# Performance work log

Hardware: AMD Instinct MI355X
Metric: run time of the kernel (lower is better)

## Reference

```python
import jax, jax.numpy as jnp
import numpy as np

C = 256          # in_channels == out_channels
L = 131072       # sequence length (multiple of BL)
BL = 64          # dilation == sliding-attention block length
CQ = C // 2      # q/k channels (r1=2)
CV = C // 2      # v channels (r2=2)
ALPHA = 1.0
EPS_IN = 1e-5    # InstanceNorm eps


def setup_inputs() -> dict:
    key = jax.random.key(0)
    ks = jax.random.split(key, 16)
    s = 0.05
    return {
        "x": jax.random.normal(ks[0], (1, C, L), jnp.float32),
        "f": jax.random.normal(ks[1], (1, C, L), jnp.float32),
        "mask": jnp.ones((1, 1, L), jnp.float32),
        # ConvFeedForward: Conv1d(C, C, 3, padding=BL, dilation=BL)
        "Wff": jax.random.normal(ks[2], (C, C, 3), jnp.float32) * s,
        "bff": jax.random.normal(ks[3], (C,), jnp.float32) * s,
        # AttLayer 1x1 convs
        "Wq": jax.random.normal(ks[4], (CQ, C), jnp.float32) * s,
        "bq": jax.random.normal(ks[5], (CQ,), jnp.float32) * s,
        "Wk": jax.random.normal(ks[6], (CQ, C), jnp.float32) * s,
        "bk": jax.random.normal(ks[7], (CQ,), jnp.float32) * s,
        "Wv": jax.random.normal(ks[8], (CV, C), jnp.float32) * s,
        "bv": jax.random.normal(ks[9], (CV,), jnp.float32) * s,
        "Wo": jax.random.normal(ks[10], (C, CV), jnp.float32) * s,
        "bo": jax.random.normal(ks[11], (C,), jnp.float32) * s,
        # AttModule.conv_1x1
        "Wc": jax.random.normal(ks[12], (C, C), jnp.float32) * s,
        "bc": jax.random.normal(ks[13], (C,), jnp.float32) * s,
    }


def _conv1x1(W, b, x):  # x: (B, Cin, L)
    return jnp.einsum('oc,bcl->bol', W, x) + b[None, :, None]


def _forward(x, f, mask, Wff, bff, Wq, bq, Wk, bk, Wv, bv, Wo, bo, Wc, bc):
    # --- ConvFeedForward: dilated conv + ReLU (same-length output) ---
    out = jax.lax.conv_general_dilated(
        x, Wff, window_strides=(1,), padding=[(BL, BL)], rhs_dilation=(BL,),
        dimension_numbers=('NCH', 'OIH', 'NCH')) + bff[None, :, None]
    out = jax.nn.relu(out)  # (1, C, L)

    # --- InstanceNorm1d (affine=False, biased var) ---
    mu = out.mean(axis=-1, keepdims=True)
    var = out.var(axis=-1, keepdims=True)
    xn = (out - mu) * jax.lax.rsqrt(var + EPS_IN)

    # --- AttLayer (sliding_att, decoder: value from f) ---
    q = _conv1x1(Wq, bq, xn)   # (1, CQ, L)
    k = _conv1x1(Wk, bk, xn)   # (1, CQ, L)
    v = _conv1x1(Wv, bv, f)    # (1, CV, L)

    nb = L // BL
    half = BL // 2
    pm = mask[:, 0:1, :]                         # (1,1,L) padding mask
    # pad halo of BL//2 zeros on each side of k, v, padding_mask
    kp = jnp.pad(k, ((0, 0), (0, 0), (half, half)))
    vp = jnp.pad(v, ((0, 0), (0, 0), (half, half)))
    mp = jnp.pad(pm, ((0, 0), (0, 0), (half, half)))
    # window index: block i sees [i*BL, i*BL + 2*BL) of the padded sequence
    idx = jnp.arange(nb)[:, None] * BL + jnp.arange(2 * BL)[None, :]  # (nb, 2BL)
    kw = kp[:, :, idx]   # (1, CQ, nb, 2BL)
    vw = vp[:, :, idx]   # (1, CV, nb, 2BL)
    mw = mp[:, 0, idx]   # (1, nb, 2BL)

    # window mask: query i attends keys [i, i+BL) within the 2BL window
    d = jnp.arange(2 * BL)[None, :] - jnp.arange(BL)[:, None]
    wm = ((d >= 0) & (d < BL)).astype(x.dtype)          # (BL, 2BL)
    fm = wm[None, None] * mw[:, :, None, :]             # (1, nb, BL, 2BL)

    qb = q.reshape(1, CQ, nb, BL)
    energy = jnp.einsum('bcnl,bcnm->bnlm', qb, kw) / np.sqrt(CQ).astype(x.dtype)
    att = jax.nn.softmax(energy + jnp.log(fm + 1e-6), axis=-1) * fm
    ov = jnp.einsum('bcnm,bnlm->bcnl', vw, att)         # (1, CV, nb, BL)
    oo = jnp.einsum('oc,bcnl->bonl', Wo, jax.nn.relu(ov)) + bo[None, :, None, None]
    att_out = oo.reshape(1, C, L) * pm                  # (1, C, L)

    # --- scaled residual + 1x1 conv + (dropout=identity) + masked residual ---
    h = ALPHA * att_out + out
    h = _conv1x1(Wc, bc, h)
    return (x + h) * mask


def reference(x, f, mask, Wff, bff, Wq, bq, Wk, bk, Wv, bv, Wo, bo, Wc, bc):
    return _forward(x, f, mask, Wff, bff, Wq, bq, Wk, bk, Wv, bv, Wo, bo, Wc, bc)
```

## Files before the change

kernel.cpp:

```cpp
#include <hip/hip_runtime.h>

#define L_LEN 131072
#define NB    2048
#define NT    1024

typedef unsigned short u16;
typedef __attribute__((ext_vector_type(4))) float f32x4;
typedef __attribute__((ext_vector_type(8))) short s16x8;
typedef __attribute__((ext_vector_type(4))) short s16x4;

#define WS_OUTT  0ull
#define WS_QT    67108864ull
#define WS_PSUM  100663296ull
#define WS_PSQ   101711872ull
#define WS_MEAN  102760448ull
#define WS_RSTD  102761472ull
#define WS_WFFB  102762496ull
#define WS_WQKB  103155712ull
#define WS_WVB   103286784ull
#define WS_WOB   103352320ull
#define WS_WCB   103417856ull
#define WS_BQKP  103548928ull

__device__ __forceinline__ u16 f2bf(float v){
  union { float f; unsigned u; } a; a.f = v;
  unsigned r = a.u + 0x7fffu + ((a.u >> 16) & 1u);
  return (u16)(r >> 16);
}
__device__ __forceinline__ float bf2f(u16 u){
  union { unsigned u; float f; } a; a.u = ((unsigned)u) << 16; return a.f;
}
__device__ __forceinline__ f32x4 mfma16(s16x8 a, s16x8 b, f32x4 c){
  return __builtin_amdgcn_mfma_f32_16x16x32_bf16(a, b, c, 0, 0, 0);
}
__device__ __forceinline__ s16x8 ld8(const void* p){ return *(const s16x8*)p; }

__global__ __launch_bounds__(256) void k_prep(
    const float* __restrict__ Wff, const float* __restrict__ Wv,
    const float* __restrict__ Wo,  const float* __restrict__ Wc,
    short* __restrict__ wffb, short* __restrict__ wvb,
    short* __restrict__ wob,  short* __restrict__ wcb)
{
  int i = blockIdx.x * 256 + threadIdx.x;
  if (i < 196608){
    int o = i / 768, kk = i % 768;
    int t = kk >> 8, c = kk & 255;
    wffb[i] = (short)f2bf(Wff[(o*256 + c)*3 + t]);
  } else if (i < 229376){ int j = i - 196608; wvb[j] = (short)f2bf(Wv[j]); }
  else if (i < 262144){ int j = i - 229376; wob[j] = (short)f2bf(Wo[j]); }
  else if (i < 327680){ int j = i - 262144; wcb[j] = (short)f2bf(Wc[j]); }
}

__global__ __launch_bounds__(512, 4) void k_conv(
    const float* __restrict__ x, const short* __restrict__ wffb,
    const float* __restrict__ bff, u16* __restrict__ outT,
    float* __restrict__ psum, float* __restrict__ psq)
{
  __shared__ u16 bl[128*40];
  const int wg = blockIdx.x, l0 = wg * 128;
  const int tid = threadIdx.x;
  const int w = tid >> 6, lane = tid & 63, p = lane & 15, g = lane >> 4;
  const int cS = tid >> 4, posq = tid & 15;
  f32x4 acc[2][8] = {};
  #pragma unroll 1
  for (int ks = 0; ks < 24; ++ks){
    const int t = ks >> 3, c0 = (ks & 7) * 32;
    {
      const int gbase = l0 + 64*(t-1) + posq*8;
      float vv[8];
      if (gbase >= 0 && gbase <= L_LEN - 8){
        const f32x4* sp = (const f32x4*)(x + (size_t)(c0 + cS)*L_LEN + gbase);
        f32x4 a0 = sp[0], a1 = sp[1];
        vv[0]=a0[0];vv[1]=a0[1];vv[2]=a0[2];vv[3]=a0[3];
        vv[4]=a1[0];vv[5]=a1[1];vv[6]=a1[2];vv[7]=a1[3];
      } else {
        #pragma unroll
        for (int u = 0; u < 8; ++u) vv[u] = 0.f;
      }
      const int col = cS ^ ((posq & 3) << 3);
      #pragma unroll
      for (int u = 0; u < 8; ++u) bl[(posq*8 + u)*40 + col] = f2bf(vv[u]);
    }
    __syncthreads();
    s16x8 af[2];
    af[0] = ld8(wffb + (size_t)(32*w +      p)*768 + ks*32 + 8*g);
    af[1] = ld8(wffb + (size_t)(32*w + 16 + p)*768 + ks*32 + 8*g);
    #pragma unroll
    for (int fn = 0; fn < 8; ++fn){
      const int r = 16*fn + p;
      s16x8 b = ld8(&bl[r*40 + ((8*g) ^ (((r>>3)&3)<<3))]);
      acc[0][fn] = mfma16(af[0], b, acc[0][fn]);
      acc[1][fn] = mfma16(af[1], b, acc[1][fn]);
    }
    __syncthreads();
  }
  #pragma unroll
  for (int fm = 0; fm < 2; ++fm){
    const int o0 = 32*w + 16*fm + 4*g;
    float ssum[4] = {0,0,0,0}, ssq[4] = {0,0,0,0};
    #pragma unroll
    for (int fn = 0; fn < 8; ++fn){
      s16x4 pk;
      #pragma unroll
      for (int i = 0; i < 4; ++i){
        float val = fmaxf(acc[fm][fn][i] + bff[o0+i], 0.f);
        pk[i] = (short)f2bf(val);
        ssum[i] += val; ssq[i] += val*val;
      }
      *(s16x4*)(outT + (size_t)(l0 + 16*fn + p)*256 + o0) = pk;
    }
    #pragma unroll
    for (int i = 0; i < 4; ++i){
      float a = ssum[i], b = ssq[i];
      #pragma unroll
      for (int d = 1; d < 16; d <<= 1){ a += __shfl_xor(a, d, 16); b += __shfl_xor(b, d, 16); }
      if (p == 0){ psum[(size_t)(o0+i)*NT + wg] = a; psq[(size_t)(o0+i)*NT + wg] = b; }
    }
  }
}

__global__ __launch_bounds__(256) void k_stats(
    const float* __restrict__ psum, const float* __restrict__ psq,
    float* __restrict__ mean, float* __restrict__ rstd)
{
  __shared__ float ss[256], sq[256];
  const int ch = blockIdx.x, tid = threadIdx.x;
  float a = 0.f, b = 0.f;
  for (int j = tid; j < NT; j += 256){ a += psum[(size_t)ch*NT + j]; b += psq[(size_t)ch*NT + j]; }
  ss[tid] = a; sq[tid] = b;
  __syncthreads();
  for (int st = 128; st > 0; st >>= 1){
    if (tid < st){ ss[tid] += ss[tid+st]; sq[tid] += sq[tid+st]; }
    __syncthreads();
  }
  if (tid == 0){
    float m = ss[0] / (float)L_LEN;
    float v = sq[0] / (float)L_LEN - m*m;
    mean[ch] = m;
    rstd[ch] = rsqrtf(v + 1e-5f);
  }
}

__global__ __launch_bounds__(256) void k_adj(
    const float* __restrict__ Wq, const float* __restrict__ Wk,
    const float* __restrict__ bq, const float* __restrict__ bk,
    const float* __restrict__ mean, const float* __restrict__ rstd,
    short* __restrict__ wqkb, float* __restrict__ bqkp)
{
  __shared__ float red[256];
  const int o = blockIdx.x, c = threadIdx.x;
  const float* src = (o < 128) ? (Wq + (size_t)o*256) : (Wk + (size_t)(o-128)*256);
  const float bias = (o < 128) ? bq[o] : bk[o-128];
  float wv = src[c] * rstd[c];
  wqkb[o*256 + c] = (short)f2bf(wv);
  red[c] = wv * mean[c];
  __syncthreads();
  for (int st = 128; st > 0; st >>= 1){
    if (c < st) red[c] += red[c+st];
    __syncthreads();
  }
  if (c == 0) bqkp[o] = bias - red[0];
}

__global__ __launch_bounds__(256, 4) void k_v(
    const float* __restrict__ fin, const short* __restrict__ wvb,
    const float* __restrict__ bv, u16* __restrict__ vout)
{
  __shared__ u16 bl[128*40];
  const int wg = blockIdx.x, l0 = wg * 128;
  const int tid = threadIdx.x;
  const int w = tid >> 6, lane = tid & 63, p = lane & 15, g = lane >> 4;
  const int posq = tid & 15;
  f32x4 acc[2][8] = {};
  #pragma unroll 1
  for (int ks = 0; ks < 8; ++ks){
    #pragma unroll
    for (int rep = 0; rep < 2; ++rep){
      const int c = rep*16 + (tid >> 4);
      const f32x4* sp = (const f32x4*)(fin + (size_t)(ks*32 + c)*L_LEN + l0 + posq*8);
      f32x4 a0 = sp[0], a1 = sp[1];
      float vv[8] = {a0[0],a0[1],a0[2],a0[3],a1[0],a1[1],a1[2],a1[3]};
      const int col = c ^ ((posq & 3) << 3);
      #pragma unroll
      for (int u = 0; u < 8; ++u) bl[(posq*8 + u)*40 + col] = f2bf(vv[u]);
    }
    __syncthreads();
    s16x8 af[2];
    af[0] = ld8(wvb + (size_t)(32*w +      p)*256 + ks*32 + 8*g);
    af[1] = ld8(wvb + (size_t)(32*w + 16 + p)*256 + ks*32 + 8*g);
    #pragma unroll
    for (int fn = 0; fn < 8; ++fn){
      const int r = 16*fn + p;
      s16x8 b = ld8(&bl[r*40 + ((8*g) ^ (((r>>3)&3)<<3))]);
      acc[0][fn] = mfma16(af[0], b, acc[0][fn]);
      acc[1][fn] = mfma16(af[1], b, acc[1][fn]);
    }
    __syncthreads();
  }
  #pragma unroll
  for (int fm = 0; fm < 2; ++fm){
    #pragma unroll
    for (int fn = 0; fn < 8; ++fn){
      #pragma unroll
      for (int i = 0; i < 4; ++i){
        const int cv = 32*w + 16*fm + 4*g + i;
        vout[(size_t)cv*L_LEN + l0 + 16*fn + p] = f2bf(acc[fm][fn][i] + bv[cv]);
      }
    }
  }
}

__global__ __launch_bounds__(512, 4) void k_qk(
    const u16* __restrict__ outT, const short* __restrict__ wqkb,
    const float* __restrict__ bqkp, u16* __restrict__ qT, u16* __restrict__ kT)
{
  extern __shared__ u16 tile[];
  const int wg = blockIdx.x, l0 = wg * 128;
  const int tid = threadIdx.x;
  const int w = tid >> 6, lane = tid & 63, p = lane & 15, g = lane >> 4;
  #pragma unroll
  for (int rep = 0; rep < 8; ++rep){
    const int idx = rep*512 + tid;
    const int r = idx >> 5, cc = idx & 31;
    s16x8 vput = ld8(outT + (size_t)(l0 + r)*256 + cc*8);
    *(s16x8*)(&tile[r*256 + ((cc*8) ^ ((r&7)<<3))]) = vput;
  }
  __syncthreads();
  f32x4 acc[2][8] = {};
  #pragma unroll
  for (int kk = 0; kk < 8; ++kk){
    s16x8 af[2];
    af[0] = ld8(wqkb + (size_t)(32*w +      p)*256 + 32*kk + 8*g);
    af[1] = ld8(wqkb + (size_t)(32*w + 16 + p)*256 + 32*kk + 8*g);
    #pragma unroll
    for (int fn = 0; fn < 8; ++fn){
      const int r = 16*fn + p;
      s16x8 b = ld8(&tile[r*256 + ((32*kk + 8*g) ^ ((r&7)<<3))]);
      acc[0][fn] = mfma16(af[0], b, acc[0][fn]);
      acc[1][fn] = mfma16(af[1], b, acc[1][fn]);
    }
  }
  #pragma unroll
  for (int fm = 0; fm < 2; ++fm){
    const int R0 = 32*w + 16*fm + 4*g;
    #pragma unroll
    for (int fn = 0; fn < 8; ++fn){
      s16x4 pk;
      #pragma unroll
      for (int i = 0; i < 4; ++i) pk[i] = (short)f2bf(acc[fm][fn][i] + bqkp[R0+i]);
      const size_t row = (size_t)(l0 + 16*fn + p);
      if (R0 < 128) *(s16x4*)(qT + row*128 + R0)       = pk;
      else          *(s16x4*)(kT + row*128 + R0 - 128) = pk;
    }
  }
}

__global__ __launch_bounds__(256, 4) void k_attn(
    const u16* __restrict__ qT, const u16* __restrict__ kT,
    const u16* __restrict__ vg, const short* __restrict__ wob,
    const float* __restrict__ bo, const float* __restrict__ mask,
    u16* __restrict__ outT, u16* __restrict__ rovg )
{
  __shared__ u16 klds[16384];
  __shared__ float maskw[128];
  const int tid = threadIdx.x;
  const int w = tid >> 6, lane = tid & 63, p = lane & 15, g = lane >> 4;
  const int n = blockIdx.x, s = n * 64;
  const float SCALE = 0.08838834764831845f;

  #pragma unroll
  for (int rep = 0; rep < 8; ++rep){
    const int idx = rep*256 + tid;
    const int m = idx >> 4, cc = idx & 15;
    const int gpos = s - 32 + m;
    s16x8 vput = {};
    if (gpos >= 0 && gpos < L_LEN) vput = ld8(kT + (size_t)gpos*128 + cc*8);
    *(s16x8*)(&klds[m*128 + ((cc*8) ^ ((m&7)<<3))]) = vput;
  }
  if (tid < 128){
    const int gp = s - 32 + tid;
    maskw[tid] = (gp >= 0 && gp < L_LEN) ? mask[gp] : 0.f;
  }
  __syncthreads();

  f32x4 e[8] = {};
  #pragma unroll
  for (int kk = 0; kk < 4; ++kk){
    s16x8 aq = ld8(qT + (size_t)(s + 16*w + p)*128 + 32*kk + 8*g);
    #pragma unroll
    for (int fn = 0; fn < 8; ++fn){
      const int m = 16*fn + p;
      s16x8 b = ld8(&klds[m*128 + ((32*kk + 8*g) ^ ((m&7)<<3))]);
      e[fn] = mfma16(aq, b, e[fn]);
    }
  }
  float M[4] = {-1e30f,-1e30f,-1e30f,-1e30f};
  float S[4] = {0.f,0.f,0.f,0.f};
  #pragma unroll
  for (int fn = 0; fn < 8; ++fn){
    #pragma unroll
    for (int i = 0; i < 4; ++i){
      const int mm = 16*fn + p;
      const int l_ = 16*w + 4*g + i;
      const int d = mm - l_;
      const float fmv = (d >= 0 && d < 64) ? maskw[mm] : 0.f;
      const float z = e[fn][i]*SCALE + __logf(fmv + 1e-6f);
      e[fn][i] = z;
      M[i] = fmaxf(M[i], z);
    }
  }
  #pragma unroll
  for (int i = 0; i < 4; ++i){
    #pragma unroll
    for (int d = 1; d < 16; d <<= 1) M[i] = fmaxf(M[i], __shfl_xor(M[i], d, 16));
  }
  #pragma unroll
  for (int fn = 0; fn < 8; ++fn){
    #pragma unroll
    for (int i = 0; i < 4; ++i){
      const float pv = __expf(e[fn][i] - M[i]);
      e[fn][i] = pv;
      S[i] += pv;
    }
  }
  #pragma unroll
  for (int i = 0; i < 4; ++i){
    #pragma unroll
    for (int d = 1; d < 16; d <<= 1) S[i] += __shfl_xor(S[i], d, 16);
  }
  float rinv[4];
  #pragma unroll
  for (int i = 0; i < 4; ++i) rinv[i] = 1.f / S[i];
  __syncthreads();
  #pragma unroll
  for (int fn = 0; fn < 8; ++fn){
    #pragma unroll
    for (int i = 0; i < 4; ++i){
      const int mm = 16*fn + p;
      const int l_ = 16*w + 4*g + i;
      const int d = mm - l_;
      const float fmv = (d >= 0 && d < 64) ? maskw[mm] : 0.f;
      klds[l_*128 + (mm ^ ((l_&7)<<3))] = f2bf(e[fn][i] * rinv[i] * fmv);
    }
  }
  __syncthreads();

  f32x4 accp[2][4] = {};
  #pragma unroll
  for (int kk = 0; kk < 4; ++kk){
    int gp0 = s - 32 + 32*kk + 8*g;
    gp0 = max(0, min(gp0, L_LEN - 8));
    s16x8 a0 = ld8(vg + (size_t)(32*w +      p)*L_LEN + gp0);
    s16x8 a1 = ld8(vg + (size_t)(32*w + 16 + p)*L_LEN + gp0);
    #pragma unroll
    for (int fn = 0; fn < 4; ++fn){
      const int l_ = 16*fn + p;
      s16x8 b = ld8(&klds[l_*128 + ((32*kk + 8*g) ^ ((l_&7)<<3))]);
      accp[0][fn] = mfma16(a0, b, accp[0][fn]);
      accp[1][fn] = mfma16(a1, b, accp[1][fn]);
    }
  }
  #pragma unroll
  for (int fm = 0; fm < 2; ++fm){
    #pragma unroll
    for (int fn = 0; fn < 4; ++fn){
      const int l_ = 16*fn + p;
      s16x4 pk;
      #pragma unroll
      for (int i = 0; i < 4; ++i) pk[i] = (short)f2bf(fmaxf(accp[fm][fn][i], 0.f));
      const int cv0 = 32*w + 16*fm + 4*g;
      *(s16x4*)(&klds[8192 + l_*128 + (cv0 ^ ((l_&7)<<3))]) = pk;
    }
  }
  __syncthreads();

  f32x4 acco[4][4] = {};
  #pragma unroll
  for (int kk = 0; kk < 4; ++kk){
    s16x8 a[4];
    #pragma unroll
    for (int fm = 0; fm < 4; ++fm)
      a[fm] = ld8(wob + (size_t)(64*w + 16*fm + p)*128 + 32*kk + 8*g);
    #pragma unroll
    for (int fn = 0; fn < 4; ++fn){
      const int l_ = 16*fn + p;
      s16x8 b = ld8(&klds[8192 + l_*128 + ((32*kk + 8*g) ^ ((l_&7)<<3))]);
      #pragma unroll
      for (int fm = 0; fm < 4; ++fm) acco[fm][fn] = mfma16(a[fm], b, acco[fm][fn]);
    }
  }
  #pragma unroll
  for (int fm = 0; fm < 4; ++fm){
    const int o0 = 64*w + 16*fm + 4*g;
    #pragma unroll
    for (int fn = 0; fn < 4; ++fn){
      const int l_ = 16*fn + p;
      const float pml = maskw[32 + l_];
      u16* hp = outT + (size_t)(s + l_)*256 + o0;
      s16x4 res = *(const s16x4*)hp;
      s16x4 pk;
      #pragma unroll
      for (int i = 0; i < 4; ++i){
        float hv = (acco[fm][fn][i] + bo[o0+i]) * pml + bf2f((u16)res[i]);
        pk[i] = (short)f2bf(hv);
      }
      *(s16x4*)hp = pk;
    }
  }
  (void)rovg;
}

__global__ __launch_bounds__(512, 4) void k_wc(
    const u16* __restrict__ hT, const short* __restrict__ wcb,
    const float* __restrict__ bc, const float* __restrict__ x,
    const float* __restrict__ mask, float* __restrict__ dout)
{
  extern __shared__ u16 tile[];
  const int wg = blockIdx.x, l0 = wg * 128;
  const int tid = threadIdx.x;
  const int w = tid >> 6, lane = tid & 63, p = lane & 15, g = lane >> 4;
  #pragma unroll
  for (int rep = 0; rep < 8; ++rep){
    const int idx = rep*512 + tid;
    const int r = idx >> 5, cc = idx & 31;
    s16x8 vput = ld8(hT + (size_t)(l0 + r)*256 + cc*8);
    *(s16x8*)(&tile[r*256 + ((cc*8) ^ ((r&7)<<3))]) = vput;
  }
  __syncthreads();
  f32x4 acc[2][8] = {};
  #pragma unroll
  for (int kk = 0; kk < 8; ++kk){
    s16x8 af[2];
    af[0] = ld8(wcb + (size_t)(32*w +      p)*256 + 32*kk + 8*g);
    af[1] = ld8(wcb + (size_t)(32*w + 16 + p)*256 + 32*kk + 8*g);
    #pragma unroll
    for (int fn = 0; fn < 8; ++fn){
      const int r = 16*fn + p;
      s16x8 b = ld8(&tile[r*256 + ((32*kk + 8*g) ^ ((r&7)<<3))]);
      acc[0][fn] = mfma16(af[0], b, acc[0][fn]);
      acc[1][fn] = mfma16(af[1], b, acc[1][fn]);
    }
  }
  #pragma unroll
  for (int fm = 0; fm < 2; ++fm){
    const int o0 = 32*w + 16*fm + 4*g;
    #pragma unroll
    for (int fn = 0; fn < 8; ++fn){
      const int pos = l0 + 16*fn + p;
      const float mk = mask[pos];
      #pragma unroll
      for (int i = 0; i < 4; ++i){
        const size_t idx = (size_t)(o0+i)*L_LEN + pos;
        dout[idx] = (x[idx] + acc[fm][fn][i] + bc[o0+i]) * mk;
      }
    }
  }
}

extern "C" void kernel_launch(void* const* d_in, const int* in_sizes, int n_in,
                              void* d_out, int out_size, void* d_ws, size_t ws_size,
                              hipStream_t stream)
{
  (void)in_sizes; (void)n_in; (void)out_size; (void)ws_size;
  const float* x    = (const float*)d_in[0];
  const float* f    = (const float*)d_in[1];
  const float* mask = (const float*)d_in[2];
  const float* Wff  = (const float*)d_in[3];
  const float* bff  = (const float*)d_in[4];
  const float* Wq   = (const float*)d_in[5];
  const float* bq   = (const float*)d_in[6];
  const float* Wk   = (const float*)d_in[7];
  const float* bk   = (const float*)d_in[8];
  const float* Wv   = (const float*)d_in[9];
  const float* bv   = (const float*)d_in[10];
  const float* Wo   = (const float*)d_in[11];
  const float* bo   = (const float*)d_in[12];
  const float* Wc   = (const float*)d_in[13];
  const float* bc   = (const float*)d_in[14];

  char* ws = (char*)d_ws;
  u16*   outT = (u16*)(ws + WS_OUTT);
  u16*   qT   = (u16*)(ws + WS_QT);
  float* psum = (float*)(ws + WS_PSUM);
  float* psq  = (float*)(ws + WS_PSQ);
  float* mean = (float*)(ws + WS_MEAN);
  float* rstd = (float*)(ws + WS_RSTD);
  short* wffb = (short*)(ws + WS_WFFB);
  short* wqkb = (short*)(ws + WS_WQKB);
  short* wvb  = (short*)(ws + WS_WVB);
  short* wob  = (short*)(ws + WS_WOB);
  short* wcb  = (short*)(ws + WS_WCB);
  float* bqkp = (float*)(ws + WS_BQKP);

  u16* vbuf = (u16*)d_out;
  u16* ktb  = (u16*)((char*)d_out + 33554432);

  (void)hipFuncSetAttribute((const void*)k_qk,
                            hipFuncAttributeMaxDynamicSharedMemorySize, 65536);
  (void)hipFuncSetAttribute((const void*)k_wc,
                            hipFuncAttributeMaxDynamicSharedMemorySize, 65536);

  k_prep <<<1280, 256, 0, stream>>>(Wff, Wv, Wo, Wc, wffb, wvb, wob, wcb);
  k_conv <<<NT,   512, 0, stream>>>(x, wffb, bff, outT, psum, psq);
  k_stats<<<256,  256, 0, stream>>>(psum, psq, mean, rstd);
  k_adj  <<<256,  256, 0, stream>>>(Wq, Wk, bq, bk, mean, rstd, wqkb, bqkp);
  k_v    <<<NT,   256, 0, stream>>>(f, wvb, bv, vbuf);
  k_qk   <<<NT,   512, 65536, stream>>>(outT, wqkb, bqkp, qT, ktb);
  k_attn <<<NB,   256, 0, stream>>>(qT, ktb, vbuf, wob, bo, mask, outT, qT);
  k_wc   <<<NT,   512, 65536, stream>>>(outT, wcb, bc, x, mask, (float*)d_out);
}
```

Measured before the change: 366.3 us.

## Stage shared x window per channel group and prefetch loads in conv and V kernels

```diff
diff --git a/kernel.cpp b/kernel.cpp
--- a/kernel.cpp
+++ b/kernel.cpp
@@ -30,6 +30,11 @@
 __device__ __forceinline__ float bf2f(u16 u){
   union { unsigned u; float f; } a; a.u = ((unsigned)u) << 16; return a.f;
 }
+__device__ __forceinline__ unsigned cvtpk(float a, float b){
+  unsigned r;
+  asm("v_cvt_pk_bf16_f32 %0, %1, %2" : "=v"(r) : "v"(a), "v"(b));
+  return r;
+}
 __device__ __forceinline__ f32x4 mfma16(s16x8 a, s16x8 b, f32x4 c){
   return __builtin_amdgcn_mfma_f32_16x16x32_bf16(a, b, c, 0, 0, 0);
 }
@@ -56,41 +61,52 @@
     const float* __restrict__ bff, u16* __restrict__ outT,
     float* __restrict__ psum, float* __restrict__ psq)
 {
-  __shared__ u16 bl[128*40];
+  __shared__ u16 xs[256*40];
   const int wg = blockIdx.x, l0 = wg * 128;
   const int tid = threadIdx.x;
   const int w = tid >> 6, lane = tid & 63, p = lane & 15, g = lane >> 4;
-  const int cS = tid >> 4, posq = tid & 15;
+  const int cl = tid >> 4, posq = tid & 15;
+  f32x4 pf[4];
+
+  auto issue = [&](int cg){
+    #pragma unroll
+    for (int u = 0; u < 4; ++u){
+      const int row = 64*u + 4*posq;
+      const long gp = (long)l0 - 64 + row;
+      if (gp >= 0 && gp + 4 <= L_LEN)
+        pf[u] = *(const f32x4*)(x + (size_t)(cg*32 + cl)*L_LEN + gp);
+      else
+        pf[u] = f32x4{0.f, 0.f, 0.f, 0.f};
+    }
+  };
+
+  issue(0);
   f32x4 acc[2][8] = {};
   #pragma unroll 1
-  for (int ks = 0; ks < 24; ++ks){
-    const int t = ks >> 3, c0 = (ks & 7) * 32;
-    {
-      const int gbase = l0 + 64*(t-1) + posq*8;
-      float vv[8];
-      if (gbase >= 0 && gbase <= L_LEN - 8){
-        const f32x4* sp = (const f32x4*)(x + (size_t)(c0 + cS)*L_LEN + gbase);
-        f32x4 a0 = sp[0], a1 = sp[1];
-        vv[0]=a0[0];vv[1]=a0[1];vv[2]=a0[2];vv[3]=a0[3];
-        vv[4]=a1[0];vv[5]=a1[1];vv[6]=a1[2];vv[7]=a1[3];
-      } else {
-        #pragma unroll
-        for (int u = 0; u < 8; ++u) vv[u] = 0.f;
+  for (int cg = 0; cg < 8; ++cg){
+    #pragma unroll
+    for (int u = 0; u < 4; ++u){
+      const int row = 64*u + 4*posq;
+      const unsigned r01 = cvtpk(pf[u][0], pf[u][1]);
+      const unsigned r23 = cvtpk(pf[u][2], pf[u][3]);
+      xs[(row+0)*40 + (cl ^ (8*(((row+0)>>2)&3)))] = (u16)(r01 & 0xffffu);
+      xs[(row+1)*40 + (cl ^ (8*(((row+1)>>2)&3)))] = (u16)(r01 >> 16);
+      xs[(row+2)*40 + (cl ^ (8*(((row+2)>>2)&3)))] = (u16)(r23 & 0xffffu);
+      xs[(row+3)*40 + (cl ^ (8*(((row+3)>>2)&3)))] = (u16)(r23 >> 16);
+    }
+    if (cg < 7) issue(cg + 1);
+    __syncthreads();
+    #pragma unroll
+    for (int t = 0; t < 3; ++t){
+      s16x8 a0 = ld8(wffb + (size_t)(32*w +      p)*768 + t*256 + cg*32 + 8*g);
+      s16x8 a1 = ld8(wffb + (size_t)(32*w + 16 + p)*768 + t*256 + cg*32 + 8*g);
+      #pragma unroll
+      for (int fn = 0; fn < 8; ++fn){
+        const int row = 64*t + 16*fn + p;
+        s16x8 b = ld8(&xs[row*40 + ((8*g) ^ (8*((row>>2)&3)))]);
+        acc[0][fn] = mfma16(a0, b, acc[0][fn]);
+        acc[1][fn] = mfma16(a1, b, acc[1][fn]);
       }
-      const int col = cS ^ ((posq & 3) << 3);
-      #pragma unroll
-      for (int u = 0; u < 8; ++u) bl[(posq*8 + u)*40 + col] = f2bf(vv[u]);
-    }
-    __syncthreads();
-    s16x8 af[2];
-    af[0] = ld8(wffb + (size_t)(32*w +      p)*768 + ks*32 + 8*g);
-    af[1] = ld8(wffb + (size_t)(32*w + 16 + p)*768 + ks*32 + 8*g);
-    #pragma unroll
-    for (int fn = 0; fn < 8; ++fn){
-      const int r = 16*fn + p;
-      s16x8 b = ld8(&bl[r*40 + ((8*g) ^ (((r>>3)&3)<<3))]);
-      acc[0][fn] = mfma16(af[0], b, acc[0][fn]);
-      acc[1][fn] = mfma16(af[1], b, acc[1][fn]);
     }
     __syncthreads();
   }
@@ -166,32 +182,44 @@
     const float* __restrict__ fin, const short* __restrict__ wvb,
     const float* __restrict__ bv, u16* __restrict__ vout)
 {
-  __shared__ u16 bl[128*40];
+  __shared__ u16 xs[128*40];
   const int wg = blockIdx.x, l0 = wg * 128;
   const int tid = threadIdx.x;
   const int w = tid >> 6, lane = tid & 63, p = lane & 15, g = lane >> 4;
-  const int posq = tid & 15;
+  const int cl = tid >> 3, posq = tid & 7;
+  f32x4 pf[4];
+
+  auto issue = [&](int cg){
+    #pragma unroll
+    for (int u = 0; u < 4; ++u){
+      const int row = 32*u + 4*posq;
+      pf[u] = *(const f32x4*)(fin + (size_t)(cg*32 + cl)*L_LEN + l0 + row);
+    }
+  };
+
+  issue(0);
   f32x4 acc[2][8] = {};
   #pragma unroll 1
-  for (int ks = 0; ks < 8; ++ks){
-    #pragma unroll
-    for (int rep = 0; rep < 2; ++rep){
-      const int c = rep*16 + (tid >> 4);
-      const f32x4* sp = (const f32x4*)(fin + (size_t)(ks*32 + c)*L_LEN + l0 + posq*8);
-      f32x4 a0 = sp[0], a1 = sp[1];
-      float vv[8] = {a0[0],a0[1],a0[2],a0[3],a1[0],a1[1],a1[2],a1[3]};
-      const int col = c ^ ((posq & 3) << 3);
-      #pragma unroll
-      for (int u = 0; u < 8; ++u) bl[(posq*8 + u)*40 + col] = f2bf(vv[u]);
-    }
+  for (int cg = 0; cg < 8; ++cg){
+    #pragma unroll
+    for (int u = 0; u < 4; ++u){
+      const int row = 32*u + 4*posq;
+      const unsigned r01 = cvtpk(pf[u][0], pf[u][1]);
+      const unsigned r23 = cvtpk(pf[u][2], pf[u][3]);
+      xs[(row+0)*40 + (cl ^ (8*(((row+0)>>2)&3)))] = (u16)(r01 & 0xffffu);
+      xs[(row+1)*40 + (cl ^ (8*(((row+1)>>2)&3)))] = (u16)(r01 >> 16);
+      xs[(row+2)*40 + (cl ^ (8*(((row+2)>>2)&3)))] = (u16)(r23 & 0xffffu);
+      xs[(row+3)*40 + (cl ^ (8*(((row+3)>>2)&3)))] = (u16)(r23 >> 16);
+    }
+    if (cg < 7) issue(cg + 1);
     __syncthreads();
     s16x8 af[2];
-    af[0] = ld8(wvb + (size_t)(32*w +      p)*256 + ks*32 + 8*g);
-    af[1] = ld8(wvb + (size_t)(32*w + 16 + p)*256 + ks*32 + 8*g);
-    #pragma unroll
-    for (int fn = 0; fn < 8; ++fn){
-      const int r = 16*fn + p;
-      s16x8 b = ld8(&bl[r*40 + ((8*g) ^ (((r>>3)&3)<<3))]);
+    af[0] = ld8(wvb + (size_t)(32*w +      p)*256 + cg*32 + 8*g);
+    af[1] = ld8(wvb + (size_t)(32*w + 16 + p)*256 + cg*32 + 8*g);
+    #pragma unroll
+    for (int fn = 0; fn < 8; ++fn){
+      const int row = 16*fn + p;
+      s16x8 b = ld8(&xs[row*40 + ((8*g) ^ (8*((row>>2)&3)))]);
       acc[0][fn] = mfma16(af[0], b, acc[0][fn]);
       acc[1][fn] = mfma16(af[1], b, acc[1][fn]);
     }
@@ -259,7 +287,7 @@
     const u16* __restrict__ qT, const u16* __restrict__ kT,
     const u16* __restrict__ vg, const short* __restrict__ wob,
     const float* __restrict__ bo, const float* __restrict__ mask,
-    u16* __restrict__ outT, u16* __restrict__ rovg )
+    u16* __restrict__ outT)
 {
   __shared__ u16 klds[16384];
   __shared__ float maskw[128];
@@ -407,7 +435,6 @@
       *(s16x4*)hp = pk;
     }
   }
-  (void)rovg;
 }
 
 __global__ __launch_bounds__(512, 4) void k_wc(
@@ -506,6 +533,6 @@
   k_adj  <<<256,  256, 0, stream>>>(Wq, Wk, bq, bk, mean, rstd, wqkb, bqkp);
   k_v    <<<NT,   256, 0, stream>>>(f, wvb, bv, vbuf);
   k_qk   <<<NT,   512, 65536, stream>>>(outT, wqkb, bqkp, qT, ktb);
-  k_attn <<<NB,   256, 0, stream>>>(qT, ktb, vbuf, wob, bo, mask, outT, qT);
+  k_attn <<<NB,   256, 0, stream>>>(qT, ktb, vbuf, wob, bo, mask, outT);
   k_wc   <<<NT,   512, 65536, stream>>>(outT, wcb, bc, x, mask, (float*)d_out);
 }
```

Result: slower. 454.2 us (+24.0%).
